# Optimization experiments

Hardware: AMD Instinct MI355X
Metric: run time of the kernel (lower is better)

Reference implementation:

```python
import jax, jax.numpy as jnp
import numpy as np

N_NODES = 50000
N_EDGES = 1000000
H_DIM = 128
OUT_DIM = 64
N_RELS = 16  # num_bases == num_rels


def setup_inputs() -> dict:
    key = jax.random.key(0)
    ks = jax.random.split(key, 12)
    node_ids = jnp.arange(N_NODES, dtype=jnp.int64) if jax.config.jax_enable_x64 else jnp.arange(N_NODES, dtype=jnp.int32)
    src = jax.random.randint(ks[0], (N_EDGES,), 0, N_NODES)
    dst = jax.random.randint(ks[1], (N_EDGES,), 0, N_NODES)
    etype = jax.random.randint(ks[2], (N_EDGES,), 0, N_RELS)
    norm = jax.random.uniform(ks[3], (N_EDGES, 1), dtype=jnp.float32)
    s1 = 1.0 / np.sqrt(H_DIM)
    s2 = 1.0 / np.sqrt(OUT_DIM)
    emb = jax.random.normal(ks[4], (N_NODES, H_DIM), dtype=jnp.float32)
    V1 = jax.random.normal(ks[5], (N_RELS, H_DIM, H_DIM), dtype=jnp.float32) * s1
    comp1 = jax.random.normal(ks[6], (N_RELS, N_RELS), dtype=jnp.float32) * (1.0 / np.sqrt(N_RELS))
    bias1 = jnp.zeros((H_DIM,), dtype=jnp.float32)
    V2 = jax.random.normal(ks[7], (N_RELS, H_DIM, OUT_DIM), dtype=jnp.float32) * s2
    comp2 = jax.random.normal(ks[8], (N_RELS, N_RELS), dtype=jnp.float32) * (1.0 / np.sqrt(N_RELS))
    bias2 = jnp.zeros((OUT_DIM,), dtype=jnp.float32)
    return {"node_ids": node_ids, "src": src, "dst": dst, "etype": etype, "norm": norm,
            "emb": emb, "V1": V1, "comp1": comp1, "bias1": bias1,
            "V2": V2, "comp2": comp2, "bias2": bias2}


def _rel_graph_conv(x, src, dst, etype, norm, V, comp, bias, num_nodes):
    # Basis decomposition: W_r = sum_b comp[r, b] * V_b  -> [R, in, out]
    W = jnp.einsum('rb,bio->rio', comp, V)
    # Per-relation transform of all nodes: [R, N, out]
    Y = jnp.einsum('ni,rio->rno', x, W)
    # Per-edge message: gather (etype, src) then scale by norm  -> [E, out]
    m = Y[etype, src] * norm
    # Scatter-add to destination nodes
    h = jax.ops.segment_sum(m, dst, num_segments=num_nodes)
    return h + bias


def reference(node_ids, src, dst, etype, norm, emb, V1, comp1, bias1, V2, comp2, bias2):
    x = emb[node_ids]  # [N, H]
    h = jax.nn.relu(_rel_graph_conv(x, src, dst, etype, norm, V1, comp1, bias1, x.shape[0]))
    h = _rel_graph_conv(h, src, dst, etype, norm, V2, comp2, bias2, x.shape[0])
    return h
```

## Files before the change

### kernel.cpp

```cpp
#include <hip/hip_runtime.h>


typedef short bf16x8 __attribute__((ext_vector_type(8)));
typedef float f32x4 __attribute__((ext_vector_type(4)));

#define RELS 16
#define HDIM 128
#define DSTBLK 66
#define MT_P 5
#define CHUNK 32
#define MAXBINS 12288
#define MAXCH 96

__device__ inline unsigned short f2bf(float f) {
  unsigned int u = __float_as_uint(f);
  unsigned int r = u + 0x7FFFu + ((u >> 16) & 1u);
  return (unsigned short)(r >> 16);
}

__device__ inline unsigned cvtpk(float lo, float hi) {
  unsigned r;
  asm("v_cvt_pk_bf16_f32 %0, %1, %2" : "=v"(r) : "v"(lo), "v"(hi));
  return r;
}

__device__ inline void barrier_nodrain() {
  __builtin_amdgcn_sched_barrier(0);
  asm volatile("s_waitcnt lgkmcnt(0)" ::: "memory");
  __builtin_amdgcn_s_barrier();
  __builtin_amdgcn_sched_barrier(0);
}

__global__ void cvt_bf16(const float* __restrict__ in, unsigned short* __restrict__ out, int n8) {
  int i = blockIdx.x * blockDim.x + threadIdx.x;
  if (i >= n8) return;
  float4 a = ((const float4*)in)[i * 2];
  float4 b = ((const float4*)in)[i * 2 + 1];
  uint4 o;
  o.x = (unsigned)f2bf(a.x) | ((unsigned)f2bf(a.y) << 16);
  o.y = (unsigned)f2bf(a.z) | ((unsigned)f2bf(a.w) << 16);
  o.z = (unsigned)f2bf(b.x) | ((unsigned)f2bf(b.y) << 16);
  o.w = (unsigned)f2bf(b.z) | ((unsigned)f2bf(b.w) << 16);
  ((uint4*)out)[i] = o;
}

__global__ void compute_w(const float* __restrict__ comp, const float* __restrict__ V,
                          unsigned short* __restrict__ Wt, int IO) {
  int idx = blockIdx.x * blockDim.x + threadIdx.x;
  if (idx >= RELS * IO * HDIM) return;
  int k = idx & (HDIM - 1);
  int o = (idx >> 7) % IO;
  int r = idx / (IO * HDIM);
  float s = 0.f;
#pragma unroll
  for (int b = 0; b < RELS; b++)
    s = fmaf(comp[r * RELS + b], V[(size_t)b * HDIM * IO + (size_t)k * IO + o], s);
  Wt[idx] = f2bf(s);
}

__global__ void hist_bins(const int* __restrict__ dst, const int* __restrict__ etype,
                          int n, int nbins, int* __restrict__ counts) {
  __shared__ int lh[MAXBINS];
  for (int j = threadIdx.x; j < nbins; j += blockDim.x) lh[j] = 0;
  __syncthreads();
  for (int i = blockIdx.x * blockDim.x + threadIdx.x; i < n; i += gridDim.x * blockDim.x)
    atomicAdd(&lh[(dst[i] / DSTBLK) * RELS + etype[i]], 1);
  __syncthreads();
  for (int j = threadIdx.x; j < nbins; j += blockDim.x) {
    int c = lh[j];
    if (c) atomicAdd(&counts[j], c);
  }
}

__global__ void scan_offsets(const int* __restrict__ counts, int* __restrict__ offsets, int nbins) {
  __shared__ int csum[256];
  const int t = threadIdx.x;
  const int CH = (nbins + 255) / 256;
  int lo = t * CH, hi = min(lo + CH, nbins);
  int s = 0;
  for (int i = lo; i < hi; i++) s += (counts[i] + 15) & ~15;
  csum[t] = s;
  __syncthreads();
#pragma unroll
  for (int d = 1; d < 256; d <<= 1) {
    int v = (t >= d) ? csum[t - d] : 0;
    __syncthreads();
    csum[t] += v;
    __syncthreads();
  }
  int run = (t == 0) ? 0 : csum[t - 1];
  for (int i = lo; i < hi; i++) {
    offsets[i] = run;
    run += (counts[i] + 15) & ~15;
  }
  if (lo < nbins && hi == nbins) offsets[nbins] = run;
}

__global__ void scatter_bins(const int* __restrict__ src, const int* __restrict__ dst,
                             const int* __restrict__ etype, const float* __restrict__ norm,
                             int n, const int* __restrict__ offsets, int* __restrict__ cursor,
                             uint2* __restrict__ ebuf) {
  for (int i = blockIdx.x * blockDim.x + threadIdx.x; i < n; i += gridDim.x * blockDim.x) {
    int d = dst[i];
    int blk = d / DSTBLK;
    int b = blk * RELS + etype[i];
    int p = offsets[b] + atomicAdd(&cursor[b], 1);
    ebuf[p] = make_uint2((unsigned)src[i] | ((unsigned)(d - blk * DSTBLK) << 20),
                         __float_as_uint(norm[i]));
  }
}

#define PHASE(CB, iE0, iE1, iG0, iG1, iH, oE0, oE1, oG0, oG1, oH, PDW)          \
  {                                                                             \
    int2 dc = descS[ci];                                                        \
    const int nRows = dc.y & 0xFF;                                              \
    const int rel = dc.y >> 8;                                                  \
    if (rel != curRel) {                                                        \
      curRel = rel;                                                             \
      const unsigned short* Wr = Wt + (size_t)rel * OUT * HDIM;                 \
      _Pragma("unroll") for (int ks = 0; ks < 4; ks++)                          \
          _Pragma("unroll") for (int nt = 0; nt < NT; nt++)                     \
              wf[ks][nt] = *(const bf16x8*)(Wr +                                \
                  (size_t)(colBase + nt * 16 + l16) * HDIM + ks * 32 + quad * 8); \
    }                                                                           \
    int2 d3 = (ci + 3 < nCh) ? descS[ci + 3] : make_int2(0, 0);                 \
    const int n3 = d3.y & 0xFF;                                                 \
    if (r0 < n3) oE0 = ebuf[d3.x + r0];                                         \
    if (16 + r0 < n3) oE1 = ebuf[d3.x + 16 + r0];                               \
    if (isHandler && myCol < n2) oH = ebuf[descS[ci + 2].x + myCol];            \
    f32x4 dacc[2][NT] = {};                                                     \
    _Pragma("unroll") for (int mt = 0; mt < 2; mt++) {                          \
      if (mt * 16 < nRows) {                                                    \
        __builtin_amdgcn_s_setprio(1);                                          \
        _Pragma("unroll") for (int ks = 0; ks < 4; ks++) {                      \
          bf16x8 a = *(const bf16x8*)&xs[CB][mt * 16 + l16][ks * 32 + quad * 8]; \
          _Pragma("unroll") for (int nt = 0; nt < NT; nt++)                     \
              dacc[mt][nt] = __builtin_amdgcn_mfma_f32_16x16x32_bf16(           \
                  a, wf[ks][nt], dacc[mt][nt], 0, 0, 0);                        \
        }                                                                       \
        __builtin_amdgcn_s_setprio(0);                                          \
      }                                                                         \
    }                                                                           \
    if (r0 < n2) oG0 = *(const uint4*)(Xb + (size_t)(iE0.x & 0xFFFFFu) * HDIM + k8 * 8); \
    if (16 + r0 < n2) oG1 = *(const uint4*)(Xb + (size_t)(iE1.x & 0xFFFFFu) * HDIM + k8 * 8); \
    {                                                                           \
      bf16x8 bfv[NT];                                                           \
      _Pragma("unroll") for (int nt = 0; nt < NT; nt++) {                       \
        uint4 bw;                                                               \
        bw.x = cvtpk(dacc[0][nt][0], dacc[0][nt][1]);                           \
        bw.y = cvtpk(dacc[0][nt][2], dacc[0][nt][3]);                           \
        bw.z = cvtpk(dacc[1][nt][0], dacc[1][nt][1]);                           \
        bw.w = cvtpk(dacc[1][nt][2], dacc[1][nt][3]);                           \
        bfv[nt] = *(bf16x8*)&bw;                                                \
      }                                                                         \
      __builtin_amdgcn_s_setprio(1);                                            \
      _Pragma("unroll") for (int mt = 0; mt < MT_P; mt++) {                     \
        bf16x8 a = *(const bf16x8*)&pmat[CB][mt * 16 + l16][quad * 8];          \
        _Pragma("unroll") for (int nt = 0; nt < NT; nt++)                       \
            pacc[mt][nt] = __builtin_amdgcn_mfma_f32_16x16x32_bf16(             \
                a, bfv[nt], pacc[mt][nt], 0, 0, 0);                             \
      }                                                                         \
      __builtin_amdgcn_s_setprio(0);                                            \
    }                                                                           \
    if (r0 < n1) *(uint4*)&xs[CB ^ 1][r0][k8 * 8] = iG0;                        \
    if (16 + r0 < n1) *(uint4*)&xs[CB ^ 1][16 + r0][k8 * 8] = iG1;              \
    if (isHandler) {                                                            \
      if (PDW >= 0) pmat[CB ^ 1][PDW][hslot] = 0;                               \
      if (myCol < n1) {                                                         \
        int dl = (int)(iH.x >> 20) & 127;                                       \
        pmat[CB ^ 1][dl][hslot] = f2bf(__uint_as_float(iH.y));                  \
        PDW = dl;                                                               \
      } else {                                                                  \
        PDW = -1;                                                               \
      }                                                                         \
    }                                                                           \
    if (ci + 1 < nCh) barrier_nodrain();                                        \
    n1 = n2; n2 = n3; ci++;                                                     \
  }

template <int OUT, bool BF16_RELU_OUT>
__launch_bounds__(256, (OUT == 64) ? 4 : 3)
__global__ void rgcn_layer(const unsigned short* __restrict__ Xb,
                           const unsigned short* __restrict__ Wt,
                           const uint2* __restrict__ ebuf,
                           const int* __restrict__ offsets, const int* __restrict__ counts,
                           const float* __restrict__ bias, void* __restrict__ Hout,
                           int nNodes) {
  constexpr int NT = OUT / 64;
  __shared__ __align__(16) unsigned short xs[2][CHUNK][136];
  __shared__ __align__(16) unsigned short pmat[2][80][40];
  __shared__ __align__(8) int2 descS[MAXCH];
  __shared__ int sBase[16], sCnt[16], sStart[17];

  const int t = threadIdx.x;
  const int w = t >> 6;
  const int lane = t & 63;
  const int quad = lane >> 4;
  const int l16 = lane & 15;
  const int r0 = t >> 4;
  const int k8 = t & 15;
  const bool isHandler = (t & 7) == 0;
  const int myCol = t >> 3;
  const int hslot = ((myCol >> 2) & 3) * 8 + ((myCol >> 4) & 1) * 4 + (myCol & 3);
  const int nodeBase = blockIdx.x * DSTBLK;
  const int binBase = blockIdx.x * RELS;
  const int colBase = w * (OUT / 4);

  for (int i = t; i < 2 * CHUNK * 136 / 8; i += 256) ((uint4*)xs)[i] = make_uint4(0, 0, 0, 0);
  for (int i = t; i < 2 * 80 * 40 / 8; i += 256) ((uint4*)pmat)[i] = make_uint4(0, 0, 0, 0);

  if (t < 16) {
    sBase[t] = offsets[binBase + t];
    sCnt[t] = counts[binBase + t];
  }
  __syncthreads();
  if (t == 0) {
    int run = 0;
#pragma unroll
    for (int b = 0; b < 16; b++) {
      sStart[b] = run;
      run += (sCnt[b] + CHUNK - 1) / CHUNK;
    }
    sStart[16] = min(run, MAXCH);
  }
  __syncthreads();
  if (t < 16) {
    int st = sStart[t], ba = sBase[t], c = sCnt[t];
    for (int j = 0; j * CHUNK < c; j++)
      if (st + j < MAXCH)
        descS[st + j] = make_int2(ba + j * CHUNK, min(CHUNK, c - j * CHUNK) | (t << 8));
  }
  __syncthreads();
  const int nCh = sStart[16];

  f32x4 pacc[MT_P][NT] = {};

  uint2 qE0, qE1, pE0, pE1;
  uint4 qG0, qG1, pG0, pG1;
  uint2 qH, pH;
  int pd0 = -1, pd1 = -1;
  int n1 = 0, n2 = 0;

  if (nCh > 0) {
    int2 d0 = descS[0];
    int2 d1 = (nCh > 1) ? descS[1] : make_int2(0, 0);
    int2 d2 = (nCh > 2) ? descS[2] : make_int2(0, 0);
    const int rows0 = d0.y & 0xFF;
    n1 = d1.y & 0xFF;
    n2 = d2.y & 0xFF;
    uint2 a0, a1, am, e10, e11;
    if (r0 < rows0) a0 = ebuf[d0.x + r0];
    if (16 + r0 < rows0) a1 = ebuf[d0.x + 16 + r0];
    if (isHandler && myCol < rows0) am = ebuf[d0.x + myCol];
    if (r0 < n1) e10 = ebuf[d1.x + r0];
    if (16 + r0 < n1) e11 = ebuf[d1.x + 16 + r0];
    if (isHandler && myCol < n1) qH = ebuf[d1.x + myCol];
    if (r0 < n2) qE0 = ebuf[d2.x + r0];
    if (16 + r0 < n2) qE1 = ebuf[d2.x + 16 + r0];
    if (r0 < rows0)
      *(uint4*)&xs[0][r0][k8 * 8] =
          *(const uint4*)(Xb + (size_t)(a0.x & 0xFFFFFu) * HDIM + k8 * 8);
    if (16 + r0 < rows0)
      *(uint4*)&xs[0][16 + r0][k8 * 8] =
          *(const uint4*)(Xb + (size_t)(a1.x & 0xFFFFFu) * HDIM + k8 * 8);
    if (isHandler && myCol < rows0) {
      int dl = (int)(am.x >> 20) & 127;
      pmat[0][dl][hslot] = f2bf(__uint_as_float(am.y));
      pd0 = dl;
    }
    if (r0 < n1) qG0 = *(const uint4*)(Xb + (size_t)(e10.x & 0xFFFFFu) * HDIM + k8 * 8);
    if (16 + r0 < n1) qG1 = *(const uint4*)(Xb + (size_t)(e11.x & 0xFFFFFu) * HDIM + k8 * 8);
  }
  barrier_nodrain();

  int curRel = -1;
  bf16x8 wf[4][NT];

  int ci = 0;
  while (ci < nCh) {
    PHASE(0, qE0, qE1, qG0, qG1, qH, pE0, pE1, pG0, pG1, pH, pd1)
    if (ci >= nCh) break;
    PHASE(1, pE0, pE1, pG0, pG1, pH, qE0, qE1, qG0, qG1, qH, pd0)
  }

#pragma unroll
  for (int mt = 0; mt < MT_P; mt++) {
#pragma unroll
    for (int reg = 0; reg < 4; reg++) {
      int ld = mt * 16 + quad * 4 + reg;
      int node = nodeBase + ld;
      if (ld < DSTBLK && node < nNodes) {
#pragma unroll
        for (int nt = 0; nt < NT; nt++) {
          int col = colBase + nt * 16 + l16;
          float v = pacc[mt][nt][reg] + bias[col];
          if constexpr (BF16_RELU_OUT)
            ((unsigned short*)Hout)[(size_t)node * OUT + col] = f2bf(fmaxf(v, 0.f));
          else
            ((float*)Hout)[(size_t)node * OUT + col] = v;
        }
      }
    }
  }
}

extern "C" void kernel_launch(void* const* d_in, const int* in_sizes, int n_in,
                              void* d_out, int out_size, void* d_ws, size_t ws_size,
                              hipStream_t stream) {
  const int*   src   = (const int*)d_in[1];
  const int*   dst   = (const int*)d_in[2];
  const int*   etype = (const int*)d_in[3];
  const float* norm  = (const float*)d_in[4];
  const float* emb   = (const float*)d_in[5];
  const float* V1    = (const float*)d_in[6];
  const float* comp1 = (const float*)d_in[7];
  const float* bias1 = (const float*)d_in[8];
  const float* V2    = (const float*)d_in[9];
  const float* comp2 = (const float*)d_in[10];
  const float* bias2 = (const float*)d_in[11];
  float* out = (float*)d_out;

  const int N = in_sizes[0];
  const int E = in_sizes[1];
  const int H = 128, O = 64;
  const int NB = (N + DSTBLK - 1) / DSTBLK;
  const int NBINS = NB * RELS;
  const int EPAD_MAX = E + NBINS * 16;

  char* ws = (char*)d_ws;
  size_t off = 0;
  auto alloc = [&](size_t bytes) -> void* {
    void* p = ws + off;
    off += (bytes + 255) & ~(size_t)255;
    return p;
  };
  unsigned short* W1t  = (unsigned short*)alloc(sizeof(short) * RELS * H * H);
  unsigned short* W2t  = (unsigned short*)alloc(sizeof(short) * RELS * O * H);
  unsigned short* embh = (unsigned short*)alloc(sizeof(short) * (size_t)N * H);
  unsigned short* h1b  = (unsigned short*)alloc(sizeof(short) * (size_t)N * H);
  uint2* ebuf = (uint2*)alloc(sizeof(uint2) * EPAD_MAX);
  int* counts  = (int*)alloc(sizeof(int) * NBINS);
  int* cursor  = (int*)alloc(sizeof(int) * NBINS);
  int* offsets = (int*)alloc(sizeof(int) * (NBINS + 1));

  hipMemsetAsync(counts, 0, sizeof(int) * NBINS, stream);
  hipMemsetAsync(cursor, 0, sizeof(int) * NBINS, stream);

  cvt_bf16<<<((size_t)N * H / 8 + 255) / 256, 256, 0, stream>>>(emb, embh, N * H / 8);
  compute_w<<<(RELS * H * H + 255) / 256, 256, 0, stream>>>(comp1, V1, W1t, H);
  compute_w<<<(RELS * O * H + 255) / 256, 256, 0, stream>>>(comp2, V2, W2t, O);
  hist_bins<<<256, 256, 0, stream>>>(dst, etype, E, NBINS, counts);
  scan_offsets<<<1, 256, 0, stream>>>(counts, offsets, NBINS);
  scatter_bins<<<1024, 256, 0, stream>>>(src, dst, etype, norm, E, offsets, cursor, ebuf);

  rgcn_layer<128, true><<<NB, 256, 0, stream>>>(embh, W1t, ebuf, offsets, counts, bias1, (void*)h1b, N);
  rgcn_layer<64, false><<<NB, 256, 0, stream>>>(h1b, W2t, ebuf, offsets, counts, bias2, (void*)out, N);
}
```

Before: 425.4 us.

## Halve rgcn_layer block to two waves and shorten gather prefetch pipeline

Each rgcn_layer block now runs with 128 threads (two waves) instead of 256. Each wave covers half the output columns, so it holds twice as many MFMA tiles and weight fragments, and each thread gathers four source rows per chunk instead of two. The prefetch pipeline is cut from three stages to two: the node-feature gathers for the next chunk are issued at the start of the phase, before the MFMAs, instead of one phase ahead. The change trades fewer waves and less latency hiding for less per-block setup and barrier overhead. It also raises register pressure under the new launch bound of 2.

```diff
diff --git a/kernel.cpp b/kernel.cpp
--- a/kernel.cpp
+++ b/kernel.cpp
@@ -110,7 +110,7 @@
   }
 }
 
-#define PHASE(CB, iE0, iE1, iG0, iG1, iH, oE0, oE1, oG0, oG1, oH, PDW)          \
+#define PHASE(CB, iE0, iE1, iE2, iE3, oE0, oE1, oE2, oE3, PDW)                  \
   {                                                                             \
     int2 dc = descS[ci];                                                        \
     const int nRows = dc.y & 0xFF;                                              \
@@ -123,11 +123,21 @@
               wf[ks][nt] = *(const bf16x8*)(Wr +                                \
                   (size_t)(colBase + nt * 16 + l16) * HDIM + ks * 32 + quad * 8); \
     }                                                                           \
-    int2 d3 = (ci + 3 < nCh) ? descS[ci + 3] : make_int2(0, 0);                 \
-    const int n3 = d3.y & 0xFF;                                                 \
-    if (r0 < n3) oE0 = ebuf[d3.x + r0];                                         \
-    if (16 + r0 < n3) oE1 = ebuf[d3.x + 16 + r0];                               \
-    if (isHandler && myCol < n2) oH = ebuf[descS[ci + 2].x + myCol];            \
+    int2 dN = (ci + 1 < nCh) ? descS[ci + 1] : make_int2(0, 0);                 \
+    int2 dN2 = (ci + 2 < nCh) ? descS[ci + 2] : make_int2(0, 0);                \
+    const int n1 = dN.y & 0xFF;                                                 \
+    const int n2 = dN2.y & 0xFF;                                                \
+    if (r0 < n2) oE0 = ebuf[dN2.x + r0];                                        \
+    if (8 + r0 < n2) oE1 = ebuf[dN2.x + 8 + r0];                                \
+    if (16 + r0 < n2) oE2 = ebuf[dN2.x + 16 + r0];                              \
+    if (24 + r0 < n2) oE3 = ebuf[dN2.x + 24 + r0];                              \
+    uint4 g0, g1, g2, g3;                                                       \
+    if (r0 < n1) g0 = *(const uint4*)(Xb + (size_t)(iE0.x & 0xFFFFFu) * HDIM + k8 * 8); \
+    if (8 + r0 < n1) g1 = *(const uint4*)(Xb + (size_t)(iE1.x & 0xFFFFFu) * HDIM + k8 * 8); \
+    if (16 + r0 < n1) g2 = *(const uint4*)(Xb + (size_t)(iE2.x & 0xFFFFFu) * HDIM + k8 * 8); \
+    if (24 + r0 < n1) g3 = *(const uint4*)(Xb + (size_t)(iE3.x & 0xFFFFFu) * HDIM + k8 * 8); \
+    uint2 hN;                                                                   \
+    if (isHandler && myCol < n1) hN = ebuf[dN.x + myCol];                       \
     f32x4 dacc[2][NT] = {};                                                     \
     _Pragma("unroll") for (int mt = 0; mt < 2; mt++) {                          \
       if (mt * 16 < nRows) {                                                    \
@@ -141,8 +151,6 @@
         __builtin_amdgcn_s_setprio(0);                                          \
       }                                                                         \
     }                                                                           \
-    if (r0 < n2) oG0 = *(const uint4*)(Xb + (size_t)(iE0.x & 0xFFFFFu) * HDIM + k8 * 8); \
-    if (16 + r0 < n2) oG1 = *(const uint4*)(Xb + (size_t)(iE1.x & 0xFFFFFu) * HDIM + k8 * 8); \
     {                                                                           \
       bf16x8 bfv[NT];                                                           \
       _Pragma("unroll") for (int nt = 0; nt < NT; nt++) {                       \
@@ -162,31 +170,33 @@
       }                                                                         \
       __builtin_amdgcn_s_setprio(0);                                            \
     }                                                                           \
-    if (r0 < n1) *(uint4*)&xs[CB ^ 1][r0][k8 * 8] = iG0;                        \
-    if (16 + r0 < n1) *(uint4*)&xs[CB ^ 1][16 + r0][k8 * 8] = iG1;              \
+    if (r0 < n1) *(uint4*)&xs[CB ^ 1][r0][k8 * 8] = g0;                         \
+    if (8 + r0 < n1) *(uint4*)&xs[CB ^ 1][8 + r0][k8 * 8] = g1;                 \
+    if (16 + r0 < n1) *(uint4*)&xs[CB ^ 1][16 + r0][k8 * 8] = g2;               \
+    if (24 + r0 < n1) *(uint4*)&xs[CB ^ 1][24 + r0][k8 * 8] = g3;               \
     if (isHandler) {                                                            \
       if (PDW >= 0) pmat[CB ^ 1][PDW][hslot] = 0;                               \
       if (myCol < n1) {                                                         \
-        int dl = (int)(iH.x >> 20) & 127;                                       \
-        pmat[CB ^ 1][dl][hslot] = f2bf(__uint_as_float(iH.y));                  \
+        int dl = (int)(hN.x >> 20) & 127;                                       \
+        pmat[CB ^ 1][dl][hslot] = f2bf(__uint_as_float(hN.y));                  \
         PDW = dl;                                                               \
       } else {                                                                  \
         PDW = -1;                                                               \
       }                                                                         \
     }                                                                           \
     if (ci + 1 < nCh) barrier_nodrain();                                        \
-    n1 = n2; n2 = n3; ci++;                                                     \
+    ci++;                                                                       \
   }
 
 template <int OUT, bool BF16_RELU_OUT>
-__launch_bounds__(256, (OUT == 64) ? 4 : 3)
+__launch_bounds__(128, 2)
 __global__ void rgcn_layer(const unsigned short* __restrict__ Xb,
                            const unsigned short* __restrict__ Wt,
                            const uint2* __restrict__ ebuf,
                            const int* __restrict__ offsets, const int* __restrict__ counts,
                            const float* __restrict__ bias, void* __restrict__ Hout,
                            int nNodes) {
-  constexpr int NT = OUT / 64;
+  constexpr int NT = OUT / 32;
   __shared__ __align__(16) unsigned short xs[2][CHUNK][136];
   __shared__ __align__(16) unsigned short pmat[2][80][40];
   __shared__ __align__(8) int2 descS[MAXCH];
@@ -199,15 +209,15 @@
   const int l16 = lane & 15;
   const int r0 = t >> 4;
   const int k8 = t & 15;
-  const bool isHandler = (t & 7) == 0;
-  const int myCol = t >> 3;
+  const bool isHandler = (t & 3) == 0;
+  const int myCol = t >> 2;
   const int hslot = ((myCol >> 2) & 3) * 8 + ((myCol >> 4) & 1) * 4 + (myCol & 3);
   const int nodeBase = blockIdx.x * DSTBLK;
   const int binBase = blockIdx.x * RELS;
-  const int colBase = w * (OUT / 4);
-
-  for (int i = t; i < 2 * CHUNK * 136 / 8; i += 256) ((uint4*)xs)[i] = make_uint4(0, 0, 0, 0);
-  for (int i = t; i < 2 * 80 * 40 / 8; i += 256) ((uint4*)pmat)[i] = make_uint4(0, 0, 0, 0);
+  const int colBase = w * (OUT / 2);
+
+  for (int i = t; i < 2 * CHUNK * 136 / 8; i += 128) ((uint4*)xs)[i] = make_uint4(0, 0, 0, 0);
+  for (int i = t; i < 2 * 80 * 40 / 8; i += 128) ((uint4*)pmat)[i] = make_uint4(0, 0, 0, 0);
 
   if (t < 16) {
     sBase[t] = offsets[binBase + t];
@@ -235,41 +245,41 @@
 
   f32x4 pacc[MT_P][NT] = {};
 
-  uint2 qE0, qE1, pE0, pE1;
-  uint4 qG0, qG1, pG0, pG1;
-  uint2 qH, pH;
+  uint2 qE0, qE1, qE2, qE3, pE0, pE1, pE2, pE3;
   int pd0 = -1, pd1 = -1;
-  int n1 = 0, n2 = 0;
 
   if (nCh > 0) {
     int2 d0 = descS[0];
     int2 d1 = (nCh > 1) ? descS[1] : make_int2(0, 0);
-    int2 d2 = (nCh > 2) ? descS[2] : make_int2(0, 0);
     const int rows0 = d0.y & 0xFF;
-    n1 = d1.y & 0xFF;
-    n2 = d2.y & 0xFF;
-    uint2 a0, a1, am, e10, e11;
+    const int n1p = d1.y & 0xFF;
+    uint2 a0, a1, a2, a3, am;
     if (r0 < rows0) a0 = ebuf[d0.x + r0];
-    if (16 + r0 < rows0) a1 = ebuf[d0.x + 16 + r0];
+    if (8 + r0 < rows0) a1 = ebuf[d0.x + 8 + r0];
+    if (16 + r0 < rows0) a2 = ebuf[d0.x + 16 + r0];
+    if (24 + r0 < rows0) a3 = ebuf[d0.x + 24 + r0];
     if (isHandler && myCol < rows0) am = ebuf[d0.x + myCol];
-    if (r0 < n1) e10 = ebuf[d1.x + r0];
-    if (16 + r0 < n1) e11 = ebuf[d1.x + 16 + r0];
-    if (isHandler && myCol < n1) qH = ebuf[d1.x + myCol];
-    if (r0 < n2) qE0 = ebuf[d2.x + r0];
-    if (16 + r0 < n2) qE1 = ebuf[d2.x + 16 + r0];
+    if (r0 < n1p) qE0 = ebuf[d1.x + r0];
+    if (8 + r0 < n1p) qE1 = ebuf[d1.x + 8 + r0];
+    if (16 + r0 < n1p) qE2 = ebuf[d1.x + 16 + r0];
+    if (24 + r0 < n1p) qE3 = ebuf[d1.x + 24 + r0];
     if (r0 < rows0)
       *(uint4*)&xs[0][r0][k8 * 8] =
           *(const uint4*)(Xb + (size_t)(a0.x & 0xFFFFFu) * HDIM + k8 * 8);
+    if (8 + r0 < rows0)
+      *(uint4*)&xs[0][8 + r0][k8 * 8] =
+          *(const uint4*)(Xb + (size_t)(a1.x & 0xFFFFFu) * HDIM + k8 * 8);
     if (16 + r0 < rows0)
       *(uint4*)&xs[0][16 + r0][k8 * 8] =
-          *(const uint4*)(Xb + (size_t)(a1.x & 0xFFFFFu) * HDIM + k8 * 8);
+          *(const uint4*)(Xb + (size_t)(a2.x & 0xFFFFFu) * HDIM + k8 * 8);
+    if (24 + r0 < rows0)
+      *(uint4*)&xs[0][24 + r0][k8 * 8] =
+          *(const uint4*)(Xb + (size_t)(a3.x & 0xFFFFFu) * HDIM + k8 * 8);
     if (isHandler && myCol < rows0) {
       int dl = (int)(am.x >> 20) & 127;
       pmat[0][dl][hslot] = f2bf(__uint_as_float(am.y));
       pd0 = dl;
     }
-    if (r0 < n1) qG0 = *(const uint4*)(Xb + (size_t)(e10.x & 0xFFFFFu) * HDIM + k8 * 8);
-    if (16 + r0 < n1) qG1 = *(const uint4*)(Xb + (size_t)(e11.x & 0xFFFFFu) * HDIM + k8 * 8);
   }
   barrier_nodrain();
 
@@ -278,9 +288,9 @@
 
   int ci = 0;
   while (ci < nCh) {
-    PHASE(0, qE0, qE1, qG0, qG1, qH, pE0, pE1, pG0, pG1, pH, pd1)
+    PHASE(0, qE0, qE1, qE2, qE3, pE0, pE1, pE2, pE3, pd1)
     if (ci >= nCh) break;
-    PHASE(1, pE0, pE1, pG0, pG1, pH, qE0, qE1, qG0, qG1, qH, pd0)
+    PHASE(1, pE0, pE1, pE2, pE3, qE0, qE1, qE2, qE3, pd0)
   }
 
 #pragma unroll
@@ -353,6 +363,6 @@
   scan_offsets<<<1, 256, 0, stream>>>(counts, offsets, NBINS);
   scatter_bins<<<1024, 256, 0, stream>>>(src, dst, etype, norm, E, offsets, cursor, ebuf);
 
-  rgcn_layer<128, true><<<NB, 256, 0, stream>>>(embh, W1t, ebuf, offsets, counts, bias1, (void*)h1b, N);
-  rgcn_layer<64, false><<<NB, 256, 0, stream>>>(h1b, W2t, ebuf, offsets, counts, bias2, (void*)out, N);
-}
+  rgcn_layer<128, true><<<NB, 128, 0, stream>>>(embh, W1t, ebuf, offsets, counts, bias1, (void*)h1b, N);
+  rgcn_layer<64, false><<<NB, 128, 0, stream>>>(h1b, W2t, ebuf, offsets, counts, bias2, (void*)out, N);
+}
```

After: 666.3 us. 1.57x slower.
